# Kernel optimization log

Hardware: AMD Instinct MI355X
Metric: run time of the kernel (lower is better)

The kernel has to match this reference:

```python
import jax, jax.numpy as jnp
import numpy as np
from jax import lax

B, N, DIM, H, HD = 4, 8192, 256, 8, 32
INTERNAL = H * HD  # 256
SCALE = HD ** -0.5


def rotate_every_two(x):
    x1 = x[..., ::2]
    x2 = x[..., 1::2]
    return jnp.stack([-x2, x1], axis=-1).reshape(x.shape)


def theta_shift(x, sin, cos):
    # sin/cos: (N, HD) broadcast against (B, H, N, HD)
    return x * cos + rotate_every_two(x) * sin


def setup_inputs() -> dict:
    key = jax.random.key(0)
    ks = jax.random.split(key, 8)
    x = jax.random.normal(ks[0], (B, N, DIM), jnp.float32)
    sin = jax.random.uniform(ks[1], (N, HD), jnp.float32)
    cos = jax.random.uniform(ks[2], (N, HD), jnp.float32)
    W_qkvo = jax.random.normal(ks[3], (4 * INTERNAL, DIM), jnp.float32) * 0.02
    b_qkvo = jnp.zeros((4 * INTERNAL,), jnp.float32)
    W_lepe = jax.random.normal(ks[4], (INTERNAL, 1, 3), jnp.float32) * 0.1  # depthwise conv (O, I/g=1, K)
    b_lepe = jnp.zeros((INTERNAL,), jnp.float32)
    W_proj = jax.random.normal(ks[5], (DIM, INTERNAL), jnp.float32) * 0.02
    b_proj = jnp.zeros((DIM,), jnp.float32)
    return {"x": x, "sin": sin, "cos": cos, "W_qkvo": W_qkvo, "b_qkvo": b_qkvo,
            "W_lepe": W_lepe, "b_lepe": b_lepe, "W_proj": W_proj, "b_proj": b_proj}


def reference(x, sin, cos, W_qkvo, b_qkvo, W_lepe, b_lepe, W_proj, b_proj):
    # qkvo projection and chunk
    qkvo = x @ W_qkvo.T + b_qkvo  # (B, N, 4*INTERNAL)
    q, k, v, o = jnp.split(qkvo, 4, axis=-1)

    # depthwise conv LEPE branch on v: (B, C, N)
    v_t = jnp.transpose(v, (0, 2, 1))
    lepe = lax.conv_general_dilated(
        v_t, W_lepe, window_strides=(1,), padding=[(1, 1)],
        dimension_numbers=("NCH", "OIH", "NCH"), feature_group_count=INTERNAL)
    lepe_out = jnp.transpose(lepe + b_lepe[None, :, None], (0, 2, 1))  # (B, N, INTERNAL)

    # split heads: (B, H, N, HD)
    def heads(t):
        return jnp.transpose(t.reshape(B, N, H, HD), (0, 2, 1, 3))
    qh, kh, vh = heads(q), heads(k), heads(v)

    qh = jax.nn.elu(qh) + 1.0
    kh = jax.nn.elu(kh) + 1.0

    # z: (B, H, N, 1) against per-head k mean
    kmean = kh.mean(axis=2, keepdims=True)  # (B, H, 1, HD)
    z = jnp.einsum("bhnd,bhmd->bhnm", qh, kmean) * SCALE

    qs = theta_shift(qh, sin, cos)
    ks_ = theta_shift(kh, sin, cos)

    s = (SCALE / N) ** 0.5
    kv_state = jnp.einsum("bhnd,bhne->bhde", ks_ * s, vh * s)  # (B, H, HD, HD)
    attn_out = jnp.einsum("bhnd,bhde->bhne", qs, kv_state)     # (B, H, N, HD)

    v_mean = vh.mean(axis=2, keepdims=True)  # (B, H, 1, HD)
    res = attn_out * (1.0 + 1.0 / (z + 1e-6)) - z * v_mean

    res = jnp.transpose(res, (0, 2, 1, 3)).reshape(B, N, INTERNAL)
    res = res + lepe_out
    return (res * o) @ W_proj.T + b_proj
```

## Files before the change

kernel.cpp:

```cpp
#include <hip/hip_runtime.h>
#include <hip/hip_bf16.h>


typedef __bf16 bf16x8 __attribute__((ext_vector_type(8)));
typedef float  f32x4  __attribute__((ext_vector_type(4)));
typedef float  f32x2  __attribute__((ext_vector_type(2)));

#define NSEQ  8192
#define TOK   32768
#define SCALE_F 0.17677669529663687f
#define S2_F    2.1579674718339462e-05f

__device__ __forceinline__ bf16x8 ld8(const __bf16* p) { return *(const bf16x8*)p; }
__device__ __forceinline__ bf16x8 ld8(const float* p) {
  f32x4 a = *(const f32x4*)p;
  f32x4 b = *(const f32x4*)(p + 4);
  bf16x8 r;
  r[0]=(__bf16)a.x; r[1]=(__bf16)a.y; r[2]=(__bf16)a.z; r[3]=(__bf16)a.w;
  r[4]=(__bf16)b.x; r[5]=(__bf16)b.y; r[6]=(__bf16)b.z; r[7]=(__bf16)b.w;
  return r;
}

template<int EPI, typename TA, typename TB, typename TO>
__global__ __launch_bounds__(256)
void gemm_kernel(const TA* __restrict__ A, const TB* __restrict__ Bw,
                 const float* __restrict__ bias,
                 TO* __restrict__ o0, __bf16* __restrict__ o1,
                 __bf16* __restrict__ o2, __bf16* __restrict__ o3)
{
  constexpr int K = 256;
  __shared__ __align__(16) __bf16 As[128*32];
  __shared__ __align__(16) __bf16 Bs[128*32];
  const int tid  = threadIdx.x;
  const int lane = tid & 63;
  const int wid  = tid >> 6;
  const int wm = wid & 1, wn = wid >> 1;
  const long m0 = (long)blockIdx.x * 128;
  const int  n0 = blockIdx.y * 128;

  const TA* ag = A  + (m0 + (tid>>2))*K + (tid&3)*8;
  const TB* bg = Bw + (long)(n0 + (tid>>2))*K + (tid&3)*8;
  __bf16* asw = As + tid*8;
  __bf16* bsw = Bs + tid*8;

  f32x4 acc[4][4] = {};

  for (int k0 = 0; k0 < K; k0 += 32) {
    bf16x8 a0 = ld8(ag + k0);
    bf16x8 a1 = ld8(ag + 64*K + k0);
    bf16x8 b0 = ld8(bg + k0);
    bf16x8 b1 = ld8(bg + 64*K + k0);
    __syncthreads();
    *(bf16x8*)asw          = a0;
    *(bf16x8*)(asw + 2048) = a1;
    *(bf16x8*)bsw          = b0;
    *(bf16x8*)(bsw + 2048) = b1;
    __syncthreads();
    const int row = lane & 15;
    const int k8  = (lane >> 4) * 8;
    bf16x8 af[4], bfr[4];
#pragma unroll
    for (int i=0;i<4;i++) af[i]  = *(const bf16x8*)&As[(wm*64 + i*16 + row)*32 + k8];
#pragma unroll
    for (int j=0;j<4;j++) bfr[j] = *(const bf16x8*)&Bs[(wn*64 + j*16 + row)*32 + k8];
#pragma unroll
    for (int i=0;i<4;i++)
#pragma unroll
      for (int j=0;j<4;j++)
        acc[i][j] = __builtin_amdgcn_mfma_f32_16x16x32_bf16(af[i], bfr[j], acc[i][j], 0,0,0);
  }

#pragma unroll
  for (int i=0;i<4;i++) {
    const long t = m0 + wm*64 + i*16 + (lane>>4)*4;
#pragma unroll
    for (int j=0;j<4;j++) {
      const int cj = n0 + wn*64 + j*16 + (lane&15);
      const float bv = bias[cj];
      if (EPI == 1) {
        const int sec = cj >> 8;
        const int c   = cj & 255;
        __bf16* dst = (sec==0)?(__bf16*)o0:(sec==1)?o1:(sec==2)?o2:o3;
#pragma unroll
        for (int r=0;r<4;r++) {
          float v = acc[i][j][r] + bv;
          if (sec < 2) v = (v > 0.f) ? (v + 1.f) : __expf(v);
          dst[(t+r)*256 + c] = (__bf16)v;
        }
      } else {
#pragma unroll
        for (int r=0;r<4;r++)
          o0[(t+r)*256 + cj] = (TO)(acc[i][j][r] + bv);
      }
    }
  }
}

__global__ __launch_bounds__(256)
void reduce_kernel(const __bf16* __restrict__ kh, const __bf16* __restrict__ vv,
                   const float* __restrict__ sing, const float* __restrict__ cosg,
                   float* __restrict__ ksum, float* __restrict__ vsum,
                   float* __restrict__ kvT)
{
  __shared__ __align__(16) float ks_s[128*32];
  __shared__ __align__(16) float v_s[128*32];
  __shared__ float ksum_s[32], vsum_s[32];
  __shared__ float kvacc[1024];
  const int tid = threadIdx.x, lane = tid & 63, wid = tid >> 6;
  const int bh = blockIdx.x;
  const int b = bh >> 3, h = bh & 7;
  const int n0 = blockIdx.y * 128;
  const long tg0 = (long)b*NSEQ + n0;
  if (tid < 32) { ksum_s[tid] = 0.f; vsum_s[tid] = 0.f; }
  for (int i = tid; i < 1024; i += 256) kvacc[i] = 0.f;
  __syncthreads();

  const int d0 = (tid & 15) * 2;
  float sk0=0.f, sk1=0.f, sv0=0.f, sv1=0.f;
  for (int i=0;i<8;i++) {
    const int nl = i*16 + (tid>>4);
    const long tg = tg0 + nl;
    const int n = n0 + nl;
    const float k0 = (float)kh[tg*256 + h*32 + d0];
    const float k1 = (float)kh[tg*256 + h*32 + d0 + 1];
    const float w0 = (float)vv[tg*256 + h*32 + d0];
    const float w1 = (float)vv[tg*256 + h*32 + d0 + 1];
    f32x2 cp = *(const f32x2*)&cosg[n*32 + d0];
    f32x2 sp = *(const f32x2*)&sing[n*32 + d0];
    ks_s[nl*32 + d0]     = k0*cp.x - k1*sp.x;
    ks_s[nl*32 + d0 + 1] = k1*cp.y + k0*sp.y;
    v_s[nl*32 + d0] = w0;  v_s[nl*32 + d0 + 1] = w1;
    sk0 += k0; sk1 += k1; sv0 += w0; sv1 += w1;
  }
  atomicAdd(&ksum_s[d0], sk0); atomicAdd(&ksum_s[d0+1], sk1);
  atomicAdd(&vsum_s[d0], sv0); atomicAdd(&vsum_s[d0+1], sv1);
  __syncthreads();

  const int db = (lane>>3)*4, eb = (lane&7)*4;
  f32x4 a0={},a1={},a2={},a3={};
  for (int nl = wid*32; nl < wid*32 + 32; nl++) {
    f32x4 kk = *(const f32x4*)&ks_s[nl*32 + db];
    f32x4 vp = *(const f32x4*)&v_s[nl*32 + eb];
    a0 += kk.x * vp;  a1 += kk.y * vp;  a2 += kk.z * vp;  a3 += kk.w * vp;
  }
#pragma unroll
  for (int e=0;e<4;e++) {
    atomicAdd(&kvacc[(eb+e)*32 + db+0], a0[e]);
    atomicAdd(&kvacc[(eb+e)*32 + db+1], a1[e]);
    atomicAdd(&kvacc[(eb+e)*32 + db+2], a2[e]);
    atomicAdd(&kvacc[(eb+e)*32 + db+3], a3[e]);
  }
  __syncthreads();
  float* dst = kvT + (long)bh*1024;
  for (int i = tid; i < 1024; i += 256) atomicAdd(&dst[i], kvacc[i]);
  if (tid < 32) { atomicAdd(&ksum[bh*32+tid], ksum_s[tid]);
                  atomicAdd(&vsum[bh*32+tid], vsum_s[tid]); }
}

__global__ __launch_bounds__(256)
void epi_kernel(const __bf16* __restrict__ qh, const __bf16* __restrict__ vv,
                const __bf16* __restrict__ oo,
                const float* __restrict__ sing, const float* __restrict__ cosg,
                const float* __restrict__ ksum, const float* __restrict__ vsum,
                const float* __restrict__ kvT,
                const float* __restrict__ Wl, const float* __restrict__ bl,
                __bf16* __restrict__ resf)
{
  __shared__ __align__(16) __bf16 qs_s[32*256];
  __shared__ __align__(16) __bf16 kv_s[8*32*32];
  __shared__ __align__(16) __bf16 lep_s[32*256];
  __shared__ float z_s[32*8];
  __shared__ float km_s[256], vm_s[256];
  const int tid = threadIdx.x, lane = tid & 63, wid = tid >> 6;
  const long t0 = (long)blockIdx.x * 32;
  const int b  = (int)(t0 >> 13);
  const int n0 = (int)(t0 & 8191);
  const int bh0 = b * 8;

  for (int i = tid; i < 8192; i += 256)
    kv_s[i] = (__bf16)(kvT[(long)bh0*1024 + i] * S2_F);
  km_s[tid] = ksum[bh0*32 + tid] * (1.f/8192.f);
  vm_s[tid] = vsum[bh0*32 + tid] * (1.f/8192.f);
  __syncthreads();

  for (int i=0;i<16;i++) {
    const int p  = i*256 + tid;
    const int t  = p >> 7;
    const int c2 = p & 127;
    const int h  = c2 >> 4;
    const int d0 = (c2 & 15) * 2;
    const long tg = t0 + t;
    const int n = n0 + t;
    const float q0 = (float)qh[tg*256 + h*32 + d0];
    const float q1 = (float)qh[tg*256 + h*32 + d0 + 1];
    f32x2 cp = *(const f32x2*)&cosg[n*32 + d0];
    f32x2 sp = *(const f32x2*)&sing[n*32 + d0];
    qs_s[t*256 + h*32 + d0]     = (__bf16)(q0*cp.x - q1*sp.x);
    qs_s[t*256 + h*32 + d0 + 1] = (__bf16)(q1*cp.y + q0*sp.y);
    float zp = q0*km_s[h*32+d0] + q1*km_s[h*32+d0+1];
    zp += __shfl_xor(zp, 1);
    zp += __shfl_xor(zp, 2);
    zp += __shfl_xor(zp, 4);
    zp += __shfl_xor(zp, 8);
    if ((lane & 15) == 0) z_s[t*8 + h] = zp * SCALE_F;
  }
  for (int i=0;i<32;i++) {
    const int f = i*256 + tid;
    const int t = f >> 8;
    const int c = f & 255;
    const long tg = t0 + t;
    const int n = n0 + t;
    const float vm1 = (n > 0)      ? (float)vv[(tg-1)*256 + c] : 0.f;
    const float v0  =                (float)vv[tg*256 + c];
    const float vp1 = (n < NSEQ-1) ? (float)vv[(tg+1)*256 + c] : 0.f;
    lep_s[f] = (__bf16)(vm1*Wl[c*3+0] + v0*Wl[c*3+1] + vp1*Wl[c*3+2] + bl[c]);
  }
  __syncthreads();

  const int e  = lane & 15;
  const int d8 = (lane >> 4) * 8;
  for (int hh=0; hh<2; hh++) {
    const int h = wid*2 + hh;
    bf16x8 bfr0 = *(const bf16x8*)&kv_s[h*1024 + e*32 + d8];
    bf16x8 bfr1 = *(const bf16x8*)&kv_s[h*1024 + (16+e)*32 + d8];
    for (int im=0; im<2; im++) {
      bf16x8 afr = *(const bf16x8*)&qs_s[(im*16 + e)*256 + h*32 + d8];
      for (int jn=0; jn<2; jn++) {
        f32x4 acc = {};
        acc = __builtin_amdgcn_mfma_f32_16x16x32_bf16(afr, jn ? bfr1 : bfr0, acc, 0,0,0);
        const int c = h*32 + jn*16 + e;
        const float vmn = vm_s[c];
#pragma unroll
        for (int r=0;r<4;r++) {
          const int t = im*16 + (lane>>4)*4 + r;
          const long tg = t0 + t;
          const float zv = z_s[t*8 + h];
          const float res = acc[r]*(1.f + 1.f/(zv + 1e-6f)) - zv*vmn
                            + (float)lep_s[t*256 + c];
          resf[tg*256 + c] = (__bf16)(res * (float)oo[tg*256 + c]);
        }
      }
    }
  }
}

extern "C" void kernel_launch(void* const* d_in, const int* in_sizes, int n_in,
                              void* d_out, int out_size, void* d_ws, size_t ws_size,
                              hipStream_t stream)
{
  const float* x    = (const float*)d_in[0];
  const float* sing = (const float*)d_in[1];
  const float* cosg = (const float*)d_in[2];
  const float* Wq   = (const float*)d_in[3];
  const float* bq   = (const float*)d_in[4];
  const float* Wl   = (const float*)d_in[5];
  const float* bl   = (const float*)d_in[6];
  const float* Wp   = (const float*)d_in[7];
  const float* bp   = (const float*)d_in[8];
  float* out = (float*)d_out;

  char* ws = (char*)d_ws;
  float*  ksum = (float*)(ws);
  float*  vsum = (float*)(ws + 4096);
  float*  kvT  = (float*)(ws + 8192);
  const size_t T0 = 256 * 1024;
  const size_t SZ = (size_t)TOK * 256 * sizeof(__bf16);
  __bf16* kh   = (__bf16*)(ws + T0);
  __bf16* vv   = (__bf16*)(ws + T0 + SZ);
  __bf16* oo   = (__bf16*)(ws + T0 + 2*SZ);
  __bf16* qh   = (__bf16*)(ws + T0 + 3*SZ);
  __bf16* resf = kh;

  hipMemsetAsync(ws, 0, 8192 + 32*1024*4, stream);

  gemm_kernel<1,float,float,__bf16><<<dim3(256, 8), 256, 0, stream>>>(x, Wq, bq, qh, kh, vv, oo);
  reduce_kernel<<<dim3(32, 64), 256, 0, stream>>>(kh, vv, sing, cosg, ksum, vsum, kvT);
  epi_kernel<<<1024, 256, 0, stream>>>(qh, vv, oo, sing, cosg, ksum, vsum, kvT, Wl, bl, resf);
  gemm_kernel<2,__bf16,float,float><<<dim3(256, 2), 256, 0, stream>>>(resf, Wp, bp, out, nullptr, nullptr, nullptr);
}
```

Measured before the change: 242.6 us.

## Store K head-major and rework reduce kernel for wider loads and fewer atomics

The QKV GEMM epilogue now writes K in a (B*H, N, 32) head-major layout, so the reduce kernel can read 16-byte contiguous vectors per token instead of scattered 2-element bf16 loads. Each reduce block now covers 512 tokens in four 128-token sub-tiles, which cuts global atomics on kvT by a factor of four. Shared tiles are padded to a stride of 36 to reduce bank conflicts. Column sums are reduced with wave shuffles before shared atomics. The risks are that the GEMM's K stores become strided per head, and the reduce grid shrinks to 512 blocks, which lowers parallelism.

Measured after the change: 225.2 us. 1.08x faster.

```diff
diff --git a/kernel.cpp b/kernel.cpp
--- a/kernel.cpp
+++ b/kernel.cpp
@@ -80,12 +80,18 @@
       if (EPI == 1) {
         const int sec = cj >> 8;
         const int c   = cj & 255;
-        __bf16* dst = (sec==0)?(__bf16*)o0:(sec==1)?o1:(sec==2)?o2:o3;
 #pragma unroll
         for (int r=0;r<4;r++) {
+          const long tt = t + r;
           float v = acc[i][j][r] + bv;
           if (sec < 2) v = (v > 0.f) ? (v + 1.f) : __expf(v);
-          dst[(t+r)*256 + c] = (__bf16)v;
+          if (sec == 1) {
+            const long bh = (tt >> 13)*8 + (c >> 5);
+            o1[(bh*8192 + (tt & 8191))*32 + (c & 31)] = (__bf16)v;
+          } else {
+            __bf16* dst = (sec==0)?(__bf16*)o0:(sec==2)?o2:o3;
+            dst[tt*256 + c] = (__bf16)v;
+          }
         }
       } else {
 #pragma unroll
@@ -97,58 +103,88 @@
 }
 
 __global__ __launch_bounds__(256)
-void reduce_kernel(const __bf16* __restrict__ kh, const __bf16* __restrict__ vv,
+void reduce_kernel(const __bf16* __restrict__ kh_t, const __bf16* __restrict__ vv,
                    const float* __restrict__ sing, const float* __restrict__ cosg,
                    float* __restrict__ ksum, float* __restrict__ vsum,
                    float* __restrict__ kvT)
 {
-  __shared__ __align__(16) float ks_s[128*32];
-  __shared__ __align__(16) float v_s[128*32];
+  __shared__ __align__(16) float ks_s[128*36];
+  __shared__ __align__(16) float v_s[128*36];
   __shared__ float ksum_s[32], vsum_s[32];
   __shared__ float kvacc[1024];
   const int tid = threadIdx.x, lane = tid & 63, wid = tid >> 6;
   const int bh = blockIdx.x;
   const int b = bh >> 3, h = bh & 7;
-  const int n0 = blockIdx.y * 128;
-  const long tg0 = (long)b*NSEQ + n0;
+  const int n0 = blockIdx.y * 512;
+  const int seg = tid & 3;
+  const int tksl = tid >> 2;
+
   if (tid < 32) { ksum_s[tid] = 0.f; vsum_s[tid] = 0.f; }
   for (int i = tid; i < 1024; i += 256) kvacc[i] = 0.f;
-  __syncthreads();
-
-  const int d0 = (tid & 15) * 2;
-  float sk0=0.f, sk1=0.f, sv0=0.f, sv1=0.f;
-  for (int i=0;i<8;i++) {
-    const int nl = i*16 + (tid>>4);
-    const long tg = tg0 + nl;
-    const int n = n0 + nl;
-    const float k0 = (float)kh[tg*256 + h*32 + d0];
-    const float k1 = (float)kh[tg*256 + h*32 + d0 + 1];
-    const float w0 = (float)vv[tg*256 + h*32 + d0];
-    const float w1 = (float)vv[tg*256 + h*32 + d0 + 1];
-    f32x2 cp = *(const f32x2*)&cosg[n*32 + d0];
-    f32x2 sp = *(const f32x2*)&sing[n*32 + d0];
-    ks_s[nl*32 + d0]     = k0*cp.x - k1*sp.x;
-    ks_s[nl*32 + d0 + 1] = k1*cp.y + k0*sp.y;
-    v_s[nl*32 + d0] = w0;  v_s[nl*32 + d0 + 1] = w1;
-    sk0 += k0; sk1 += k1; sv0 += w0; sv1 += w1;
-  }
-  atomicAdd(&ksum_s[d0], sk0); atomicAdd(&ksum_s[d0+1], sk1);
-  atomicAdd(&vsum_s[d0], sv0); atomicAdd(&vsum_s[d0+1], sv1);
-  __syncthreads();
-
+
+  float sk[8] = {}, sv[8] = {};
+  f32x4 a0={},a1={},a2={},a3={};
   const int db = (lane>>3)*4, eb = (lane&7)*4;
-  f32x4 a0={},a1={},a2={},a3={};
-  for (int nl = wid*32; nl < wid*32 + 32; nl++) {
-    f32x4 kk = *(const f32x4*)&ks_s[nl*32 + db];
-    f32x4 vp = *(const f32x4*)&v_s[nl*32 + eb];
-    a0 += kk.x * vp;  a1 += kk.y * vp;  a2 += kk.z * vp;  a3 += kk.w * vp;
-  }
+
+  for (int sub = 0; sub < 4; sub++) {
+    const int nbase = n0 + sub*128;
+    __syncthreads();
+#pragma unroll
+    for (int i=0;i<2;i++) {
+      const int tok = i*64 + tksl;
+      const int n = nbase + tok;
+      bf16x8 k8 = *(const bf16x8*)&kh_t[((long)bh*8192 + n)*32 + seg*8];
+      bf16x8 w8 = *(const bf16x8*)&vv[((long)b*8192 + n)*256 + h*32 + seg*8];
+      f32x4 cA = *(const f32x4*)&cosg[n*32 + seg*8];
+      f32x4 cB = *(const f32x4*)&cosg[n*32 + seg*8 + 4];
+      f32x4 sA = *(const f32x4*)&sing[n*32 + seg*8];
+      f32x4 sB = *(const f32x4*)&sing[n*32 + seg*8 + 4];
+      float kf[8], wf[8], cf[8], sf[8], ks[8];
+#pragma unroll
+      for (int j=0;j<8;j++) { kf[j]=(float)k8[j]; wf[j]=(float)w8[j]; }
+      cf[0]=cA.x;cf[1]=cA.y;cf[2]=cA.z;cf[3]=cA.w;cf[4]=cB.x;cf[5]=cB.y;cf[6]=cB.z;cf[7]=cB.w;
+      sf[0]=sA.x;sf[1]=sA.y;sf[2]=sA.z;sf[3]=sA.w;sf[4]=sB.x;sf[5]=sB.y;sf[6]=sB.z;sf[7]=sB.w;
+#pragma unroll
+      for (int j=0;j<8;j+=2) {
+        ks[j]   = kf[j]*cf[j]     - kf[j+1]*sf[j];
+        ks[j+1] = kf[j+1]*cf[j+1] + kf[j]*sf[j+1];
+      }
+      f32x4 q0 = {ks[0],ks[1],ks[2],ks[3]}, q1 = {ks[4],ks[5],ks[6],ks[7]};
+      *(f32x4*)&ks_s[tok*36 + seg*8]     = q0;
+      *(f32x4*)&ks_s[tok*36 + seg*8 + 4] = q1;
+      f32x4 p0 = {wf[0],wf[1],wf[2],wf[3]}, p1 = {wf[4],wf[5],wf[6],wf[7]};
+      *(f32x4*)&v_s[tok*36 + seg*8]     = p0;
+      *(f32x4*)&v_s[tok*36 + seg*8 + 4] = p1;
+#pragma unroll
+      for (int j=0;j<8;j++) { sk[j] += kf[j]; sv[j] += wf[j]; }
+    }
+    __syncthreads();
+    for (int t2 = 0; t2 < 32; t2++) {
+      const int nl = wid*32 + t2;
+      f32x4 kk = *(const f32x4*)&ks_s[nl*36 + db];
+      f32x4 vp = *(const f32x4*)&v_s[nl*36 + eb];
+      a0 += kk.x * vp;  a1 += kk.y * vp;  a2 += kk.z * vp;  a3 += kk.w * vp;
+    }
+  }
+
 #pragma unroll
   for (int e=0;e<4;e++) {
     atomicAdd(&kvacc[(eb+e)*32 + db+0], a0[e]);
     atomicAdd(&kvacc[(eb+e)*32 + db+1], a1[e]);
     atomicAdd(&kvacc[(eb+e)*32 + db+2], a2[e]);
     atomicAdd(&kvacc[(eb+e)*32 + db+3], a3[e]);
+  }
+#pragma unroll
+  for (int m = 4; m <= 32; m <<= 1) {
+#pragma unroll
+    for (int j=0;j<8;j++) { sk[j] += __shfl_xor(sk[j], m); sv[j] += __shfl_xor(sv[j], m); }
+  }
+  if (lane < 4) {
+#pragma unroll
+    for (int j=0;j<8;j++) {
+      atomicAdd(&ksum_s[lane*8 + j], sk[j]);
+      atomicAdd(&vsum_s[lane*8 + j], sv[j]);
+    }
   }
   __syncthreads();
   float* dst = kvT + (long)bh*1024;
@@ -265,16 +301,16 @@
   float*  kvT  = (float*)(ws + 8192);
   const size_t T0 = 256 * 1024;
   const size_t SZ = (size_t)TOK * 256 * sizeof(__bf16);
-  __bf16* kh   = (__bf16*)(ws + T0);
+  __bf16* kh_t = (__bf16*)(ws + T0);
   __bf16* vv   = (__bf16*)(ws + T0 + SZ);
   __bf16* oo   = (__bf16*)(ws + T0 + 2*SZ);
   __bf16* qh   = (__bf16*)(ws + T0 + 3*SZ);
-  __bf16* resf = kh;
+  __bf16* resf = kh_t;
 
   hipMemsetAsync(ws, 0, 8192 + 32*1024*4, stream);
 
-  gemm_kernel<1,float,float,__bf16><<<dim3(256, 8), 256, 0, stream>>>(x, Wq, bq, qh, kh, vv, oo);
-  reduce_kernel<<<dim3(32, 64), 256, 0, stream>>>(kh, vv, sing, cosg, ksum, vsum, kvT);
+  gemm_kernel<1,float,float,__bf16><<<dim3(256, 8), 256, 0, stream>>>(x, Wq, bq, qh, kh_t, vv, oo);
+  reduce_kernel<<<dim3(32, 16), 256, 0, stream>>>(kh_t, vv, sing, cosg, ksum, vsum, kvT);
   epi_kernel<<<1024, 256, 0, stream>>>(qh, vv, oo, sing, cosg, ksum, vsum, kvT, Wl, bl, resf);
   gemm_kernel<2,__bf16,float,float><<<dim3(256, 2), 256, 0, stream>>>(resf, Wp, bp, out, nullptr, nullptr, nullptr);
 }
```
